# Kernel tuning notes

Hardware: AMD Instinct MI355X
Metric: run time of the kernel (lower is better)

The kernel has to match this reference:

```python
import jax, jax.numpy as jnp
import numpy as np

B, S, D = 4, 2048, 1024
THETA = 10000.0


def apply_rope(x, pos):
    # x: (..., seq, d), pos: (..., seq). Interleaved-pair rotary embedding.
    d = x.shape[-1]
    inv_freq = 1.0 / (THETA ** (jnp.arange(0, d, 2, dtype=jnp.float32) / d))  # (d/2,)
    ang = pos.astype(jnp.float32)[..., None] * inv_freq                        # (..., seq, d/2)
    cos, sin = jnp.cos(ang), jnp.sin(ang)
    x1, x2 = x[..., 0::2], x[..., 1::2]
    r1 = x1 * cos - x2 * sin
    r2 = x1 * sin + x2 * cos
    return jnp.stack([r1, r2], axis=-1).reshape(x.shape)


def setup_inputs() -> dict:
    key = jax.random.key(0)
    ks = jax.random.split(key, 5)
    scale = 1.0 / np.sqrt(D)
    x = jax.random.normal(ks[0], (B, S, D), dtype=jnp.float32)
    Wq = jax.random.normal(ks[1], (D, D), dtype=jnp.float32) * scale
    Wk = jax.random.normal(ks[2], (D, D), dtype=jnp.float32) * scale
    Wv = jax.random.normal(ks[3], (D, D), dtype=jnp.float32) * scale
    Wo = jax.random.normal(ks[4], (D, D), dtype=jnp.float32) * scale
    token_positions = jnp.tile(jnp.arange(S, dtype=jnp.int64), (B, 1))
    return {"x": x, "Wq": Wq, "Wk": Wk, "Wv": Wv, "Wo": Wo,
            "token_positions": token_positions}


def reference(x, Wq, Wk, Wv, Wo, token_positions):
    # Projections (Linear stores W as (out, in); y = x @ W^T, no bias)
    Q = x @ Wq.T
    K = x @ Wk.T
    V = x @ Wv.T
    Q = apply_rope(Q, token_positions)
    K = apply_rope(K, token_positions)
    d_k = K.shape[-1]
    scores = jnp.einsum('bqd,bkd->bqk', Q, K) / jnp.sqrt(jnp.float32(d_k))
    seq = x.shape[-2]
    causal = jnp.tril(jnp.ones((seq, seq), dtype=bool))  # qi >= kj
    scores = jnp.where(causal, scores, -jnp.inf)
    weights = jax.nn.softmax(scores, axis=-1)
    attn = jnp.einsum('bqk,bkd->bqd', weights, V)
    return attn @ Wo.T
```

## Files before the change

kernel.cpp:

```cpp
#include <hip/hip_runtime.h>
#include <math.h>

constexpr int Bc = 4;
constexpr int Sc = 2048;
constexpr int Dc = 1024;

using bf16x8 = __bf16 __attribute__((ext_vector_type(8)));
using f32x4  = float  __attribute__((ext_vector_type(4)));

__device__ __forceinline__ ushort f2bf(float f) {
    uint u = __float_as_uint(f);
    u += 0x7FFFu + ((u >> 16) & 1u);
    return (ushort)(u >> 16);
}
__device__ __forceinline__ float bf2f(ushort h) {
    return __uint_as_float(((uint)h) << 16);
}

__device__ __forceinline__ void gload_lds16(const void* g, void* l) {
    __builtin_amdgcn_global_load_lds(
        (const __attribute__((address_space(1))) void*)g,
        (__attribute__((address_space(3))) void*)l, 16, 0, 0);
}

__global__ __launch_bounds__(256)
void cvt_f32_bf16_k(const float* __restrict__ src, ushort* __restrict__ dst, int n)
{
    for (long i = ((long)blockIdx.x * 256 + threadIdx.x) * 4; i < n;
         i += (long)gridDim.x * 256 * 4) {
        float4 v = *(const float4*)(src + i);
        ushort4 o;
        o.x = f2bf(v.x); o.y = f2bf(v.y); o.z = f2bf(v.z); o.w = f2bf(v.w);
        *(ushort4*)(dst + i) = o;
    }
}

enum { M_BF16 = 0, M_ROPE = 1, M_SCORES = 2, M_PV = 3, M_F32OUT = 4, M_VTRANS = 5 };

template<int MODE>
__global__ __launch_bounds__(256)
void mfma_bt_k(const ushort* __restrict__ A, const ushort* __restrict__ B,
               void* __restrict__ Cv, int M, int N, int K,
               long sA, long sB, long sC)
{
    const int bx = blockIdx.x, by = blockIdx.y, bz = blockIdx.z;
    if (MODE == M_SCORES && bx > by) return;

    A += (long)bz * sA;
    B += (long)bz * sB;

    __shared__ ushort As[128][32];
    __shared__ ushort Bs[128][32];

    const int t    = threadIdx.x;
    const int lane = t & 63;
    const int wid  = t >> 6;
    const int wr   = wid >> 1;
    const int wc   = wid & 1;

    const int srow = wid * 32 + (lane >> 2);
    const int scol = (lane & 3) * 8;
    const long abase = (long)(by * 128) * K;
    const long bbase = (long)(bx * 128) * K;

    f32x4 acc[4][4];
#pragma unroll
    for (int m = 0; m < 4; ++m)
#pragma unroll
        for (int n = 0; n < 4; ++n) acc[m][n] = (f32x4){0.f, 0.f, 0.f, 0.f};

    const int kend = (MODE == M_PV) ? min(K, (by + 1) * 128) : K;

    const int fr = lane & 15;
    const int fk = (lane >> 4) * 8;

    for (int k0 = 0; k0 < kend; k0 += 32) {
        __syncthreads();
#pragma unroll
        for (int c = 0; c < 2; ++c) {
            const int r = srow + c * 16;
            gload_lds16(A + abase + (long)r * K + k0 + scol,
                        &As[wid * 32 + c * 16][0]);
            gload_lds16(B + bbase + (long)r * K + k0 + scol,
                        &Bs[wid * 32 + c * 16][0]);
        }
        __syncthreads();

        bf16x8 af[4], bfr[4];
#pragma unroll
        for (int m = 0; m < 4; ++m)
            af[m] = *(const bf16x8*)&As[wr * 64 + m * 16 + fr][fk];
#pragma unroll
        for (int n = 0; n < 4; ++n)
            bfr[n] = *(const bf16x8*)&Bs[wc * 64 + n * 16 + fr][fk];
#pragma unroll
        for (int m = 0; m < 4; ++m)
#pragma unroll
            for (int n = 0; n < 4; ++n)
                acc[m][n] = __builtin_amdgcn_mfma_f32_16x16x32_bf16(
                    af[m], bfr[n], acc[m][n], 0, 0, 0);
    }

    if constexpr (MODE == M_VTRANS) {
        __shared__ ushort Ts[128][136];
#pragma unroll
        for (int m = 0; m < 4; ++m)
#pragma unroll
            for (int n = 0; n < 4; ++n)
#pragma unroll
                for (int j = 0; j < 4; ++j) {
                    const int c_loc = wc * 64 + n * 16 + fr;
                    const int r_loc = wr * 64 + m * 16 + (lane >> 4) * 4 + j;
                    Ts[c_loc][r_loc] = f2bf(acc[m][n][j]);
                }
        __syncthreads();
        const int b  = (by * 128) >> 11;
        const int s0 = (by * 128) & (Sc - 1);
        ushort* Vt = (ushort*)Cv + (long)b * Dc * Sc;
#pragma unroll
        for (int pass = 0; pass < 8; ++pass) {
            const int ci = pass * 16 + (t >> 4);
            const int ch = t & 15;
            uint4 vv = *(const uint4*)&Ts[ci][ch * 8];
            *(uint4*)&Vt[(long)(bx * 128 + ci) * Sc + s0 + ch * 8] = vv;
        }
        return;
    }

    const int orow = by * 128 + wr * 64;
    const int ocol = bx * 128 + wc * 64;
#pragma unroll
    for (int m = 0; m < 4; ++m) {
#pragma unroll
        for (int n = 0; n < 4; ++n) {
            const int col = ocol + n * 16 + fr;
#pragma unroll
            for (int j = 0; j < 4; ++j) {
                const int row = orow + m * 16 + (lane >> 4) * 4 + j;
                float v = acc[m][n][j];
                if (MODE == M_SCORES) v *= 0.03125f;
                if (MODE == M_ROPE) {
                    float partner = __shfl_xor(v, 1);
                    const float kfac = 9.210340371976184f / 1024.0f;
                    float freq = expf(-(float)(col & ~1) * kfac);
                    float pos  = (float)(row & (Sc - 1));
                    float s, c;
                    sincosf(pos * freq, &s, &c);
                    v = (col & 1) ? fmaf(partner, s, v * c)
                                  : fmaf(-partner, s, v * c);
                }
                if (MODE == M_F32OUT) {
                    ((float*)Cv)[(long)bz * sC + (long)row * N + col] = v;
                } else {
                    ((ushort*)Cv)[(long)bz * sC + (long)row * N + col] = f2bf(v);
                }
            }
        }
    }
}

__device__ __forceinline__ float blk_reduce(float v, bool is_max, float* sm)
{
#pragma unroll
    for (int off = 32; off; off >>= 1) {
        float o = __shfl_down(v, off);
        v = is_max ? fmaxf(v, o) : (v + o);
    }
    const int lane = threadIdx.x & 63, wid = threadIdx.x >> 6;
    if (lane == 0) sm[wid] = v;
    __syncthreads();
    if (threadIdx.x == 0) {
        float r = sm[0];
        for (int w = 1; w < 4; ++w) r = is_max ? fmaxf(r, sm[w]) : (r + sm[w]);
        sm[0] = r;
    }
    __syncthreads();
    float r = sm[0];
    __syncthreads();
    return r;
}

__global__ __launch_bounds__(256)
void softmax_bf16_k(ushort* __restrict__ P, int seq)
{
    const int q = blockIdx.x, b = blockIdx.y;
    ushort* row = P + ((long)b * seq + q) * seq;
    const int valid = q + 1;
    const int t = threadIdx.x;
    __shared__ float buf[Sc];
    __shared__ float sm[4];

    for (int i = t; i < valid; i += 256) buf[i] = bf2f(row[i]);
    __syncthreads();

    float m = -1e30f;
    for (int i = t; i < valid; i += 256) m = fmaxf(m, buf[i]);
    m = blk_reduce(m, true, sm);

    float s = 0.0f;
    for (int i = t; i < valid; i += 256) {
        float e = __expf(buf[i] - m);
        buf[i] = e;
        s += e;
    }
    s = blk_reduce(s, false, sm);
    const float inv = 1.0f / s;

    for (int i = t; i < seq; i += 256)
        row[i] = (i < valid) ? f2bf(buf[i] * inv) : (ushort)0;
}

extern "C" void kernel_launch(void* const* d_in, const int* in_sizes, int n_in,
                              void* d_out, int out_size, void* d_ws, size_t ws_size,
                              hipStream_t stream)
{
    const float* x  = (const float*)d_in[0];
    const float* Wq = (const float*)d_in[1];
    const float* Wk = (const float*)d_in[2];
    const float* Wv = (const float*)d_in[3];
    const float* Wo = (const float*)d_in[4];
    float* out = (float*)d_out;

    const long MD = (long)Bc * Sc * Dc;
    const long DD = (long)Dc * Dc;

    ushort* Xb  = (ushort*)d_ws;
    ushort* Wqb = Xb  + MD;
    ushort* Wkb = Wqb + DD;
    ushort* Wvb = Wkb + DD;
    ushort* Wob = Wvb + DD;
    ushort* Qb  = Wob + DD;
    ushort* Kb  = Qb  + MD;
    ushort* Vt  = Kb  + MD;
    ushort* Pb  = Vt  + MD;
    ushort* Ab  = Pb  + (long)Bc * Sc * Sc;

    dim3 blk(256);

    cvt_f32_bf16_k<<<2048, blk, 0, stream>>>(x,  Xb,  (int)MD);
    cvt_f32_bf16_k<<<1024, blk, 0, stream>>>(Wq, Wqb, (int)DD);
    cvt_f32_bf16_k<<<1024, blk, 0, stream>>>(Wk, Wkb, (int)DD);
    cvt_f32_bf16_k<<<1024, blk, 0, stream>>>(Wv, Wvb, (int)DD);
    cvt_f32_bf16_k<<<1024, blk, 0, stream>>>(Wo, Wob, (int)DD);

    const int Mall = Bc * Sc;

    dim3 gproj(Dc / 128, Mall / 128, 1);
    mfma_bt_k<M_ROPE>  <<<gproj, blk, 0, stream>>>(Xb, Wqb, Qb, Mall, Dc, Dc, 0, 0, 0);
    mfma_bt_k<M_ROPE>  <<<gproj, blk, 0, stream>>>(Xb, Wkb, Kb, Mall, Dc, Dc, 0, 0, 0);
    mfma_bt_k<M_VTRANS><<<gproj, blk, 0, stream>>>(Xb, Wvb, Vt, Mall, Dc, Dc, 0, 0, 0);

    dim3 gsc(Sc / 128, Sc / 128, Bc);
    mfma_bt_k<M_SCORES><<<gsc, blk, 0, stream>>>(
        Qb, Kb, Pb, Sc, Sc, Dc, (long)Sc * Dc, (long)Sc * Dc, (long)Sc * Sc);

    dim3 gsm(Sc, Bc, 1);
    softmax_bf16_k<<<gsm, blk, 0, stream>>>(Pb, Sc);

    dim3 gpv(Dc / 128, Sc / 128, Bc);
    mfma_bt_k<M_PV><<<gpv, blk, 0, stream>>>(
        Pb, Vt, Ab, Sc, Dc, Sc, (long)Sc * Sc, (long)Dc * Sc, (long)Sc * Dc);

    mfma_bt_k<M_F32OUT><<<gproj, blk, 0, stream>>>(Ab, Wob, out, Mall, Dc, Dc, 0, 0, 0);
}
```

Before: 679.5 us.

## Fuse fp32-to-bf16 casts into GEMM loads, swizzle blocks, wave-per-row softmax

Removes the standalone fp32-to-bf16 conversion kernels by having the projection and output GEMMs load fp32 operands, convert them in registers and store bf16 into LDS. Adds a block-index swizzle that spreads consecutive tiles across 8 groups, and replaces the block-per-row softmax with a wave-per-row version that keeps a row in registers and reduces with shuffles. This saves launches and the intermediate bf16 buffers. In exchange the fp32 loads are synchronous, pass through registers and read twice the bytes per tile, and each projection reconverts x.

```diff
diff --git a/kernel.cpp b/kernel.cpp
--- a/kernel.cpp
+++ b/kernel.cpp
@@ -16,6 +16,12 @@
 __device__ __forceinline__ float bf2f(ushort h) {
     return __uint_as_float(((uint)h) << 16);
 }
+__device__ __forceinline__ uint4 pack8(float4 lo, float4 hi) {
+    ushort o[8];
+    o[0] = f2bf(lo.x); o[1] = f2bf(lo.y); o[2] = f2bf(lo.z); o[3] = f2bf(lo.w);
+    o[4] = f2bf(hi.x); o[5] = f2bf(hi.y); o[6] = f2bf(hi.z); o[7] = f2bf(hi.w);
+    return *(const uint4*)o;
+}
 
 __device__ __forceinline__ void gload_lds16(const void* g, void* l) {
     __builtin_amdgcn_global_load_lds(
@@ -23,31 +29,26 @@
         (__attribute__((address_space(3))) void*)l, 16, 0, 0);
 }
 
+enum { M_ROPE = 1, M_SCORES = 2, M_PV = 3, M_F32OUT = 4, M_VTRANS = 5 };
+
+template<int MODE, bool AF32, bool BF32>
 __global__ __launch_bounds__(256)
-void cvt_f32_bf16_k(const float* __restrict__ src, ushort* __restrict__ dst, int n)
-{
-    for (long i = ((long)blockIdx.x * 256 + threadIdx.x) * 4; i < n;
-         i += (long)gridDim.x * 256 * 4) {
-        float4 v = *(const float4*)(src + i);
-        ushort4 o;
-        o.x = f2bf(v.x); o.y = f2bf(v.y); o.z = f2bf(v.z); o.w = f2bf(v.w);
-        *(ushort4*)(dst + i) = o;
-    }
-}
-
-enum { M_BF16 = 0, M_ROPE = 1, M_SCORES = 2, M_PV = 3, M_F32OUT = 4, M_VTRANS = 5 };
-
-template<int MODE>
-__global__ __launch_bounds__(256)
-void mfma_bt_k(const ushort* __restrict__ A, const ushort* __restrict__ B,
+void mfma_bt_k(const void* __restrict__ Av, const void* __restrict__ Bv,
                void* __restrict__ Cv, int M, int N, int K,
                long sA, long sB, long sC)
 {
-    const int bx = blockIdx.x, by = blockIdx.y, bz = blockIdx.z;
+    const int gx = gridDim.x;
+    int flat = blockIdx.y * gx + blockIdx.x;
+    const int q8 = (gx * gridDim.y) >> 3;
+    flat = (flat & 7) * q8 + (flat >> 3);
+    const int bx = flat % gx, by = flat / gx, bz = blockIdx.z;
+
     if (MODE == M_SCORES && bx > by) return;
 
-    A += (long)bz * sA;
-    B += (long)bz * sB;
+    const ushort* Ab = (const ushort*)Av + (AF32 ? 0 : (long)bz * sA);
+    const ushort* Bb = (const ushort*)Bv + (BF32 ? 0 : (long)bz * sB);
+    const float*  Af = (const float*)Av;
+    const float*  Bf = (const float*)Bv;
 
     __shared__ ushort As[128][32];
     __shared__ ushort Bs[128][32];
@@ -75,14 +76,38 @@
     const int fk = (lane >> 4) * 8;
 
     for (int k0 = 0; k0 < kend; k0 += 32) {
+        float4 apre[2][2], bpre[2][2];
+        if (AF32) {
+#pragma unroll
+            for (int c = 0; c < 2; ++c) {
+                const float* s = Af + abase + (long)(srow + c * 16) * K + k0 + scol;
+                apre[c][0] = *(const float4*)s;
+                apre[c][1] = *(const float4*)(s + 4);
+            }
+        }
+        if (BF32) {
+#pragma unroll
+            for (int c = 0; c < 2; ++c) {
+                const float* s = Bf + bbase + (long)(srow + c * 16) * K + k0 + scol;
+                bpre[c][0] = *(const float4*)s;
+                bpre[c][1] = *(const float4*)(s + 4);
+            }
+        }
         __syncthreads();
 #pragma unroll
         for (int c = 0; c < 2; ++c) {
-            const int r = srow + c * 16;
-            gload_lds16(A + abase + (long)r * K + k0 + scol,
-                        &As[wid * 32 + c * 16][0]);
-            gload_lds16(B + bbase + (long)r * K + k0 + scol,
-                        &Bs[wid * 32 + c * 16][0]);
+            if (AF32)
+                *(uint4*)&As[wid * 32 + c * 16 + (lane >> 2)][scol] =
+                    pack8(apre[c][0], apre[c][1]);
+            else
+                gload_lds16(Ab + abase + (long)(srow + c * 16) * K + k0 + scol,
+                            &As[wid * 32 + c * 16][0]);
+            if (BF32)
+                *(uint4*)&Bs[wid * 32 + c * 16 + (lane >> 2)][scol] =
+                    pack8(bpre[c][0], bpre[c][1]);
+            else
+                gload_lds16(Bb + bbase + (long)(srow + c * 16) * K + k0 + scol,
+                            &Bs[wid * 32 + c * 16][0]);
         }
         __syncthreads();
 
@@ -103,6 +128,7 @@
 
     if constexpr (MODE == M_VTRANS) {
         __shared__ ushort Ts[128][136];
+        __syncthreads();
 #pragma unroll
         for (int m = 0; m < 4; ++m)
 #pragma unroll
@@ -114,15 +140,15 @@
                     Ts[c_loc][r_loc] = f2bf(acc[m][n][j]);
                 }
         __syncthreads();
-        const int b  = (by * 128) >> 11;
+        const int b  = by >> 4;
         const int s0 = (by * 128) & (Sc - 1);
-        ushort* Vt = (ushort*)Cv + (long)b * Dc * Sc;
+        ushort* Vp = (ushort*)Cv + (long)b * Dc * Sc;
 #pragma unroll
         for (int pass = 0; pass < 8; ++pass) {
             const int ci = pass * 16 + (t >> 4);
             const int ch = t & 15;
             uint4 vv = *(const uint4*)&Ts[ci][ch * 8];
-            *(uint4*)&Vt[(long)(bx * 128 + ci) * Sc + s0 + ch * 8] = vv;
+            *(uint4*)&Vp[(long)(bx * 128 + ci) * Sc + s0 + ch * 8] = vv;
         }
         return;
     }
@@ -159,55 +185,53 @@
     }
 }
 
-__device__ __forceinline__ float blk_reduce(float v, bool is_max, float* sm)
+__global__ __launch_bounds__(256)
+void softmax_wave_k(ushort* __restrict__ P)
 {
-#pragma unroll
-    for (int off = 32; off; off >>= 1) {
-        float o = __shfl_down(v, off);
-        v = is_max ? fmaxf(v, o) : (v + o);
-    }
-    const int lane = threadIdx.x & 63, wid = threadIdx.x >> 6;
-    if (lane == 0) sm[wid] = v;
-    __syncthreads();
-    if (threadIdx.x == 0) {
-        float r = sm[0];
-        for (int w = 1; w < 4; ++w) r = is_max ? fmaxf(r, sm[w]) : (r + sm[w]);
-        sm[0] = r;
-    }
-    __syncthreads();
-    float r = sm[0];
-    __syncthreads();
-    return r;
-}
-
-__global__ __launch_bounds__(256)
-void softmax_bf16_k(ushort* __restrict__ P, int seq)
-{
-    const int q = blockIdx.x, b = blockIdx.y;
-    ushort* row = P + ((long)b * seq + q) * seq;
+    const int t = threadIdx.x, lane = t & 63, w = t >> 6;
+    const long rowid = (long)blockIdx.x * 4 + w;
+    const int q = (int)(rowid & (Sc - 1));
+    ushort* row = P + rowid * Sc;
     const int valid = q + 1;
-    const int t = threadIdx.x;
-    __shared__ float buf[Sc];
-    __shared__ float sm[4];
-
-    for (int i = t; i < valid; i += 256) buf[i] = bf2f(row[i]);
-    __syncthreads();
-
+
+    float v[32];
     float m = -1e30f;
-    for (int i = t; i < valid; i += 256) m = fmaxf(m, buf[i]);
-    m = blk_reduce(m, true, sm);
-
-    float s = 0.0f;
-    for (int i = t; i < valid; i += 256) {
-        float e = __expf(buf[i] - m);
-        buf[i] = e;
-        s += e;
-    }
-    s = blk_reduce(s, false, sm);
+#pragma unroll
+    for (int c = 0; c < 4; ++c) {
+        uint4 raw = *(const uint4*)&row[c * 512 + lane * 8];
+        const ushort* rs = (const ushort*)&raw;
+#pragma unroll
+        for (int j = 0; j < 8; ++j) {
+            const int col = c * 512 + lane * 8 + j;
+            float f = bf2f(rs[j]);
+            v[c * 8 + j] = f;
+            if (col < valid) m = fmaxf(m, f);
+        }
+    }
+#pragma unroll
+    for (int off = 32; off; off >>= 1) m = fmaxf(m, __shfl_xor(m, off));
+
+    float s = 0.f;
+#pragma unroll
+    for (int c = 0; c < 4; ++c)
+#pragma unroll
+        for (int j = 0; j < 8; ++j) {
+            const int col = c * 512 + lane * 8 + j;
+            float e = (col < valid) ? __expf(v[c * 8 + j] - m) : 0.f;
+            v[c * 8 + j] = e;
+            s += e;
+        }
+#pragma unroll
+    for (int off = 32; off; off >>= 1) s += __shfl_xor(s, off);
     const float inv = 1.0f / s;
 
-    for (int i = t; i < seq; i += 256)
-        row[i] = (i < valid) ? f2bf(buf[i] * inv) : (ushort)0;
+#pragma unroll
+    for (int c = 0; c < 4; ++c) {
+        ushort o[8];
+#pragma unroll
+        for (int j = 0; j < 8; ++j) o[j] = f2bf(v[c * 8 + j] * inv);
+        *(uint4*)&row[c * 512 + lane * 8] = *(const uint4*)o;
+    }
 }
 
 extern "C" void kernel_launch(void* const* d_in, const int* in_sizes, int n_in,
@@ -222,44 +246,34 @@
     float* out = (float*)d_out;
 
     const long MD = (long)Bc * Sc * Dc;
-    const long DD = (long)Dc * Dc;
-
-    ushort* Xb  = (ushort*)d_ws;
-    ushort* Wqb = Xb  + MD;
-    ushort* Wkb = Wqb + DD;
-    ushort* Wvb = Wkb + DD;
-    ushort* Wob = Wvb + DD;
-    ushort* Qb  = Wob + DD;
-    ushort* Kb  = Qb  + MD;
-    ushort* Vt  = Kb  + MD;
-    ushort* Pb  = Vt  + MD;
-    ushort* Ab  = Pb  + (long)Bc * Sc * Sc;
-
+
+    ushort* Qb = (ushort*)d_ws;
+    ushort* Kb = Qb + MD;
+    ushort* Vt = Kb + MD;
+    ushort* Pb = Vt + MD;
+    ushort* Ab = Pb + (long)Bc * Sc * Sc;
+
+    const int Mall = Bc * Sc;
     dim3 blk(256);
 
-    cvt_f32_bf16_k<<<2048, blk, 0, stream>>>(x,  Xb,  (int)MD);
-    cvt_f32_bf16_k<<<1024, blk, 0, stream>>>(Wq, Wqb, (int)DD);
-    cvt_f32_bf16_k<<<1024, blk, 0, stream>>>(Wk, Wkb, (int)DD);
-    cvt_f32_bf16_k<<<1024, blk, 0, stream>>>(Wv, Wvb, (int)DD);
-    cvt_f32_bf16_k<<<1024, blk, 0, stream>>>(Wo, Wob, (int)DD);
-
-    const int Mall = Bc * Sc;
-
     dim3 gproj(Dc / 128, Mall / 128, 1);
-    mfma_bt_k<M_ROPE>  <<<gproj, blk, 0, stream>>>(Xb, Wqb, Qb, Mall, Dc, Dc, 0, 0, 0);
-    mfma_bt_k<M_ROPE>  <<<gproj, blk, 0, stream>>>(Xb, Wkb, Kb, Mall, Dc, Dc, 0, 0, 0);
-    mfma_bt_k<M_VTRANS><<<gproj, blk, 0, stream>>>(Xb, Wvb, Vt, Mall, Dc, Dc, 0, 0, 0);
+    mfma_bt_k<M_ROPE,   true, true><<<gproj, blk, 0, stream>>>(
+        x, Wq, Qb, Mall, Dc, Dc, 0, 0, 0);
+    mfma_bt_k<M_ROPE,   true, true><<<gproj, blk, 0, stream>>>(
+        x, Wk, Kb, Mall, Dc, Dc, 0, 0, 0);
+    mfma_bt_k<M_VTRANS, true, true><<<gproj, blk, 0, stream>>>(
+        x, Wv, Vt, Mall, Dc, Dc, 0, 0, 0);
 
     dim3 gsc(Sc / 128, Sc / 128, Bc);
-    mfma_bt_k<M_SCORES><<<gsc, blk, 0, stream>>>(
+    mfma_bt_k<M_SCORES, false, false><<<gsc, blk, 0, stream>>>(
         Qb, Kb, Pb, Sc, Sc, Dc, (long)Sc * Dc, (long)Sc * Dc, (long)Sc * Sc);
 
-    dim3 gsm(Sc, Bc, 1);
-    softmax_bf16_k<<<gsm, blk, 0, stream>>>(Pb, Sc);
+    softmax_wave_k<<<2048, blk, 0, stream>>>(Pb);
 
     dim3 gpv(Dc / 128, Sc / 128, Bc);
-    mfma_bt_k<M_PV><<<gpv, blk, 0, stream>>>(
+    mfma_bt_k<M_PV,     false, false><<<gpv, blk, 0, stream>>>(
         Pb, Vt, Ab, Sc, Dc, Sc, (long)Sc * Sc, (long)Dc * Sc, (long)Sc * Dc);
 
-    mfma_bt_k<M_F32OUT><<<gproj, blk, 0, stream>>>(Ab, Wob, out, Mall, Dc, Dc, 0, 0, 0);
-}
+    mfma_bt_k<M_F32OUT, false, true><<<gproj, blk, 0, stream>>>(
+        Ab, Wo, out, Mall, Dc, Dc, 0, 0, 0);
+}
```

Result: slower. 757.1 us (+11.4%).
